# Optimization experiments

Measured on AMD Instinct MI355X. Metric: run time of the kernel, lower is better.

## Reference

```python
import jax, jax.numpy as jnp
import numpy as np

N_NODES = 50000
N_EDGES = 800000
IN_DIM = 128
OUT_DIM = 64
NEG_SLOPE = 0.2
EPS = 1e-8


def setup_inputs() -> dict:
    key = jax.random.key(0)
    k1, k2, k3, k4, k5 = jax.random.split(key, 5)
    x = jax.random.normal(k1, (N_NODES, IN_DIM), dtype=jnp.float32)
    edge_index = jax.random.randint(k2, (2, N_EDGES), 0, N_NODES, dtype=jnp.int64)
    # xavier-like scale for the linear weight
    W = jax.random.normal(k3, (IN_DIM, OUT_DIM), dtype=jnp.float32) * (1.0 / np.sqrt(IN_DIM))
    att_src = jax.random.normal(k4, (OUT_DIM,), dtype=jnp.float32) * 0.1
    att_dst = jax.random.normal(k5, (OUT_DIM,), dtype=jnp.float32) * 0.1
    bias = jnp.zeros((OUT_DIM,), dtype=jnp.float32)
    return {"x": x, "edge_index": edge_index, "W": W,
            "att_src": att_src, "att_dst": att_dst, "bias": bias}


def reference(x, edge_index, W, att_src, att_dst, bias):
    src, dst = edge_index[0], edge_index[1]
    h = x @ W                                  # (N, F_out)
    h_src = h[src]                             # (E, F_out) gather
    # per-edge score: a_src^T h_i + a_dst^T h_j
    e = h_src @ att_src + h[dst] @ att_dst     # (E,)
    e = jax.nn.leaky_relu(e, NEG_SLOPE)
    alpha = jax.nn.sigmoid(e)
    # per-dst normalization (sigmoid attention, not softmax)
    denom = jax.ops.segment_sum(alpha, dst, num_segments=N_NODES) + EPS  # (N,)
    alpha = alpha / denom[dst]
    msg = h_src * alpha[:, None]               # (E, F_out)
    out = jax.ops.segment_sum(msg, dst, num_segments=N_NODES)  # (N, F_out)
    return out + bias
```

## Files before the change

### kernel.cpp

```cpp
#include <hip/hip_runtime.h>

static constexpr int NN   = 50000;
static constexpr int NE   = 800000;
static constexpr int FIN  = 128;
static constexpr int FOUT = 64;
static constexpr int GEMM_NBLK = (NN + 63) / 64;
static constexpr int CAP  = 64;
static constexpr int NRANGE = 8;
static constexpr int RSZ  = NN / NRANGE;
static constexpr int AGG_NBLK = 2048;

static constexpr int NRG    = 196;
static constexpr int CAPSEG = 5120;
static constexpr int PA_NBLK = 98;
static constexpr int FUSE_NBLK = GEMM_NBLK + NRG;

static constexpr int WT_LD = 136;

typedef short bf16x8 __attribute__((ext_vector_type(8)));
typedef float f32x4  __attribute__((ext_vector_type(4)));

static __device__ __forceinline__ unsigned short f2bf(float f) {
    unsigned u = __float_as_uint(f);
    u += 0x7FFFu + ((u >> 16) & 1u);
    return (unsigned short)(u >> 16);
}
static __device__ __forceinline__ float bf2f(unsigned short b) {
    return __uint_as_float(((unsigned)b) << 16);
}

__global__ __launch_bounds__(1024) void k_binA(
    const int* __restrict__ src, const int* __restrict__ dst,
    int* __restrict__ rangeCursor, unsigned int* __restrict__ epack)
{
    __shared__ int hist[NRG];
    __shared__ int base[NRG];
    const int t = threadIdx.x;
    for (int i = t; i < NRG; i += 1024) hist[i] = 0;
    __syncthreads();

    const int g = blockIdx.x * 1024 + t;
    const bool act = g < NE / 8;
    int dd[8], ss[8], rk[8], bn[8];
    if (act) {
        const int4 d0 = ((const int4*)dst)[g * 2];
        const int4 d1 = ((const int4*)dst)[g * 2 + 1];
        const int4 s0 = ((const int4*)src)[g * 2];
        const int4 s1 = ((const int4*)src)[g * 2 + 1];
        dd[0]=d0.x; dd[1]=d0.y; dd[2]=d0.z; dd[3]=d0.w;
        dd[4]=d1.x; dd[5]=d1.y; dd[6]=d1.z; dd[7]=d1.w;
        ss[0]=s0.x; ss[1]=s0.y; ss[2]=s0.z; ss[3]=s0.w;
        ss[4]=s1.x; ss[5]=s1.y; ss[6]=s1.z; ss[7]=s1.w;
        #pragma unroll
        for (int u = 0; u < 8; ++u) {
            bn[u] = dd[u] >> 8;
            rk[u] = atomicAdd(&hist[bn[u]], 1);
        }
    }
    __syncthreads();
    for (int i = t; i < NRG; i += 1024)
        base[i] = hist[i] ? atomicAdd(&rangeCursor[i], hist[i]) : 0;
    __syncthreads();
    if (act) {
        #pragma unroll
        for (int u = 0; u < 8; ++u) {
            const int pos = base[bn[u]] + rk[u];
            if (pos < CAPSEG)
                epack[bn[u] * CAPSEG + pos] =
                    ((unsigned)dd[u] << 16) | (unsigned)ss[u];
        }
    }
}

__global__ __launch_bounds__(256) void k_gemm_binB(
    const float* __restrict__ x, const float* __restrict__ W,
    const float* __restrict__ att_src, const float* __restrict__ att_dst,
    unsigned short* __restrict__ hb, float* __restrict__ ssrc,
    float* __restrict__ sdst, const int* __restrict__ rangeCursor,
    const unsigned int* __restrict__ epack, int* __restrict__ counts,
    unsigned short* __restrict__ bkt)
{
    __shared__ alignas(16) unsigned short SML[64 * WT_LD + 4 * 1024];
    const int t = threadIdx.x;

    if (blockIdx.x >= GEMM_NBLK) {
        const int r = blockIdx.x - GEMM_NBLK;
        int* cur = (int*)SML;
        cur[t] = 0;
        __syncthreads();
        int nE = rangeCursor[r];
        if (nE > CAPSEG) nE = CAPSEG;
        for (int i = t; i < nE; i += 256) {
            const unsigned p = epack[r * CAPSEG + i];
            const int d16 = (int)(p >> 16);
            const int pos = atomicAdd(&cur[d16 & 255], 1);
            if (pos < CAP)
                bkt[(d16 << 6) + pos] = (unsigned short)(p & 0xFFFFu);
        }
        __syncthreads();
        const int node = (r << 8) + t;
        if (node < NN) counts[node] = cur[t];
        return;
    }

    const float4* W4 = (const float4*)W;
    for (int i = t; i < 2048; i += 256) {
        const float4 w4 = W4[i];
        const int k = i >> 4, n0 = (i & 15) << 2;
        SML[(n0+0) * WT_LD + k] = f2bf(w4.x);
        SML[(n0+1) * WT_LD + k] = f2bf(w4.y);
        SML[(n0+2) * WT_LD + k] = f2bf(w4.z);
        SML[(n0+3) * WT_LD + k] = f2bf(w4.w);
    }
    __syncthreads();

    const int wave  = t >> 6;
    const int lane  = t & 63;
    const int row16 = lane & 15;
    const int kblk  = lane >> 4;
    const int rbase = blockIdx.x * 64 + wave * 16;

    int rowA = rbase + row16; if (rowA >= NN) rowA = NN - 1;
    const float* xrow = x + (size_t)rowA * FIN;

    f32x4 acc0 = {0,0,0,0}, acc1 = {0,0,0,0}, acc2 = {0,0,0,0}, acc3 = {0,0,0,0};

    #pragma unroll
    for (int ks = 0; ks < 4; ++ks) {
        const int k0 = ks * 32 + kblk * 8;
        const float4 xa = *(const float4*)(xrow + k0);
        const float4 xb = *(const float4*)(xrow + k0 + 4);
        bf16x8 af;
        af[0] = (short)f2bf(xa.x); af[1] = (short)f2bf(xa.y);
        af[2] = (short)f2bf(xa.z); af[3] = (short)f2bf(xa.w);
        af[4] = (short)f2bf(xb.x); af[5] = (short)f2bf(xb.y);
        af[6] = (short)f2bf(xb.z); af[7] = (short)f2bf(xb.w);

        const bf16x8 b0 = *(const bf16x8*)(&SML[(0*16 + row16) * WT_LD + k0]);
        const bf16x8 b1 = *(const bf16x8*)(&SML[(1*16 + row16) * WT_LD + k0]);
        const bf16x8 b2 = *(const bf16x8*)(&SML[(2*16 + row16) * WT_LD + k0]);
        const bf16x8 b3 = *(const bf16x8*)(&SML[(3*16 + row16) * WT_LD + k0]);
        acc0 = __builtin_amdgcn_mfma_f32_16x16x32_bf16(af, b0, acc0, 0, 0, 0);
        acc1 = __builtin_amdgcn_mfma_f32_16x16x32_bf16(af, b1, acc1, 0, 0, 0);
        acc2 = __builtin_amdgcn_mfma_f32_16x16x32_bf16(af, b2, acc2, 0, 0, 0);
        acc3 = __builtin_amdgcn_mfma_f32_16x16x32_bf16(af, b3, acc3, 0, 0, 0);
    }

    float as0 = att_src[ 0 + row16], as1 = att_src[16 + row16];
    float as2 = att_src[32 + row16], as3 = att_src[48 + row16];
    float ad0 = att_dst[ 0 + row16], ad1 = att_dst[16 + row16];
    float ad2 = att_dst[32 + row16], ad3 = att_dst[48 + row16];
    #pragma unroll
    for (int reg = 0; reg < 4; ++reg) {
        float p = acc0[reg]*as0 + acc1[reg]*as1 + acc2[reg]*as2 + acc3[reg]*as3;
        float q = acc0[reg]*ad0 + acc1[reg]*ad1 + acc2[reg]*ad2 + acc3[reg]*ad3;
        #pragma unroll
        for (int m = 1; m <= 8; m <<= 1) {
            p += __shfl_xor(p, m, 64);
            q += __shfl_xor(q, m, 64);
        }
        if (row16 == 0) {
            const int r = rbase + kblk * 4 + reg;
            if (r < NN) { ssrc[r] = p; sdst[r] = q; }
        }
    }

    unsigned short* hT = SML + 64 * WT_LD + wave * 1024;
    #pragma unroll
    for (int reg = 0; reg < 4; ++reg) {
        const int rr = (kblk * 4 + reg) * 64;
        hT[rr +  0 + row16] = f2bf(acc0[reg]);
        hT[rr + 16 + row16] = f2bf(acc1[reg]);
        hT[rr + 32 + row16] = f2bf(acc2[reg]);
        hT[rr + 48 + row16] = f2bf(acc3[reg]);
    }
    __syncthreads();
    {
        const int rr = lane >> 2;
        const int cc = (lane & 3) << 4;
        const int grow = rbase + rr;
        if (grow < NN) {
            const uint4 v0 = *(const uint4*)(hT + rr * 64 + cc);
            const uint4 v1 = *(const uint4*)(hT + rr * 64 + cc + 8);
            *(uint4*)(hb + (size_t)grow * FOUT + cc)     = v0;
            *(uint4*)(hb + (size_t)grow * FOUT + cc + 8) = v1;
        }
    }
}

__global__ __launch_bounds__(256) void k_agg(
    const unsigned short* __restrict__ hb, const unsigned short* __restrict__ bkt,
    const int* __restrict__ counts, const float* __restrict__ ssrc,
    const float* __restrict__ sdst, const float* __restrict__ bias,
    float* __restrict__ out)
{
    const int r    = blockIdx.x & 7;
    const int wave = threadIdx.x >> 6;
    const int lane = threadIdx.x & 63;
    const int eq   = lane >> 3;
    const int c8   = lane & 7;
    const int c16  = c8 << 3;
    const int wstride = (AGG_NBLK >> 3) * 4;
    const float4 bLo = *(const float4*)(bias + c16);
    const float4 bHi = *(const float4*)(bias + c16 + 4);

    for (int local = (blockIdx.x >> 3) * 4 + wave; local < RSZ;
         local += 2 * wstride) {
        const int localB = local + wstride;
        const bool hasB  = localB < RSZ;
        const int nA   = r * RSZ + local;
        const int nB   = hasB ? r * RSZ + localB : nA;
        const int offA = nA << 6;
        const int offB = nB << 6;
        int cntA = counts[nA]; if (cntA > CAP) cntA = CAP;
        int cntB = hasB ? counts[nB] : 0; if (cntB > CAP) cntB = CAP;
        const float zdA = sdst[nA];
        const float zdB = sdst[nB];

        float accA[8] = {0,0,0,0,0,0,0,0};
        float accB[8] = {0,0,0,0,0,0,0,0};
        float asumA = 0.f, asumB = 0.f;

        const int nchA = (cntA + 15) >> 4;
        const int nchB = (cntB + 15) >> 4;
        const int nch  = nchA > nchB ? nchA : nchB;

        for (int c = 0; c < nch; ++c) {
            const int s0 = (c << 4) + (eq << 1);
            const unsigned wA = *(const unsigned*)(bkt + offA + s0);
            const unsigned wB = *(const unsigned*)(bkt + offB + s0);
            unsigned a0 = wA & 0xFFFFu, a1 = wA >> 16;
            unsigned b0 = wB & 0xFFFFu, b1 = wB >> 16;
            if (s0     >= cntA) a0 = 0u;
            if (s0 + 1 >= cntA) a1 = 0u;
            if (s0     >= cntB) b0 = 0u;
            if (s0 + 1 >= cntB) b1 = 0u;

            const float zA0 = ssrc[a0], zA1 = ssrc[a1];
            const float zB0 = ssrc[b0], zB1 = ssrc[b1];
            const uint4 hA0 = *(const uint4*)(hb + (size_t)a0 * FOUT + c16);
            const uint4 hA1 = *(const uint4*)(hb + (size_t)a1 * FOUT + c16);
            const uint4 hB0 = *(const uint4*)(hb + (size_t)b0 * FOUT + c16);
            const uint4 hB1 = *(const uint4*)(hb + (size_t)b1 * FOUT + c16);

            float sA0 = zA0 + zdA; sA0 = fmaxf(sA0, 0.2f * sA0);
            float sA1 = zA1 + zdA; sA1 = fmaxf(sA1, 0.2f * sA1);
            float sB0 = zB0 + zdB; sB0 = fmaxf(sB0, 0.2f * sB0);
            float sB1 = zB1 + zdB; sB1 = fmaxf(sB1, 0.2f * sB1);
            const float aA0 = (s0     < cntA) ? 1.f/(1.f+__expf(-sA0)) : 0.f;
            const float aA1 = (s0 + 1 < cntA) ? 1.f/(1.f+__expf(-sA1)) : 0.f;
            const float aB0 = (s0     < cntB) ? 1.f/(1.f+__expf(-sB0)) : 0.f;
            const float aB1 = (s0 + 1 < cntB) ? 1.f/(1.f+__expf(-sB1)) : 0.f;

            const unsigned uA0[4] = {hA0.x, hA0.y, hA0.z, hA0.w};
            const unsigned uA1[4] = {hA1.x, hA1.y, hA1.z, hA1.w};
            const unsigned uB0[4] = {hB0.x, hB0.y, hB0.z, hB0.w};
            const unsigned uB1[4] = {hB1.x, hB1.y, hB1.z, hB1.w};
            #pragma unroll
            for (int k = 0; k < 4; ++k) {
                accA[2*k]   += aA0 * bf2f((unsigned short)(uA0[k] & 0xFFFFu))
                             + aA1 * bf2f((unsigned short)(uA1[k] & 0xFFFFu));
                accA[2*k+1] += aA0 * bf2f((unsigned short)(uA0[k] >> 16))
                             + aA1 * bf2f((unsigned short)(uA1[k] >> 16));
                accB[2*k]   += aB0 * bf2f((unsigned short)(uB0[k] & 0xFFFFu))
                             + aB1 * bf2f((unsigned short)(uB1[k] & 0xFFFFu));
                accB[2*k+1] += aB0 * bf2f((unsigned short)(uB0[k] >> 16))
                             + aB1 * bf2f((unsigned short)(uB1[k] >> 16));
            }
            asumA += aA0 + aA1;
            asumB += aB0 + aB1;
        }

        #pragma unroll
        for (int m = 8; m <= 32; m <<= 1) {
            #pragma unroll
            for (int k = 0; k < 8; ++k) {
                accA[k] += __shfl_xor(accA[k], m, 64);
                accB[k] += __shfl_xor(accB[k], m, 64);
            }
            asumA += __shfl_xor(asumA, m, 64);
            asumB += __shfl_xor(asumB, m, 64);
        }

        if (eq == 0) {
            const float invA = 1.f / (asumA + 1e-8f);
            float4 lo, hi;
            lo.x = accA[0]*invA + bLo.x; lo.y = accA[1]*invA + bLo.y;
            lo.z = accA[2]*invA + bLo.z; lo.w = accA[3]*invA + bLo.w;
            hi.x = accA[4]*invA + bHi.x; hi.y = accA[5]*invA + bHi.y;
            hi.z = accA[6]*invA + bHi.z; hi.w = accA[7]*invA + bHi.w;
            *(float4*)(out + (size_t)nA * FOUT + c16)     = lo;
            *(float4*)(out + (size_t)nA * FOUT + c16 + 4) = hi;
            if (hasB) {
                const float invB = 1.f / (asumB + 1e-8f);
                lo.x = accB[0]*invB + bLo.x; lo.y = accB[1]*invB + bLo.y;
                lo.z = accB[2]*invB + bLo.z; lo.w = accB[3]*invB + bLo.w;
                hi.x = accB[4]*invB + bHi.x; hi.y = accB[5]*invB + bHi.y;
                hi.z = accB[6]*invB + bHi.z; hi.w = accB[7]*invB + bHi.w;
                *(float4*)(out + (size_t)nB * FOUT + c16)     = lo;
                *(float4*)(out + (size_t)nB * FOUT + c16 + 4) = hi;
            }
        }
    }
}

extern "C" void kernel_launch(void* const* d_in, const int* in_sizes, int n_in,
                              void* d_out, int out_size, void* d_ws, size_t ws_size,
                              hipStream_t stream)
{
    const float* x       = (const float*)d_in[0];
    const int*   ei      = (const int*)  d_in[1];
    const float* W       = (const float*)d_in[2];
    const float* att_src = (const float*)d_in[3];
    const float* att_dst = (const float*)d_in[4];
    const float* bias    = (const float*)d_in[5];
    float* out = (float*)d_out;

    unsigned short* hb  = (unsigned short*)d_ws;
    float* ssrc         = (float*)(hb + (size_t)NN * FOUT);
    float* sdst         = ssrc + NN;
    int*   counts       = (int*)(sdst + NN);
    unsigned short* bkt = (unsigned short*)(counts + NN);
    unsigned int* epack = (unsigned int*)(bkt + (size_t)NN * CAP);
    int* rangeCursor    = (int*)(epack + (size_t)NRG * CAPSEG);

    const int* src = ei;
    const int* dst = ei + NE;

    (void)hipMemsetAsync(rangeCursor, 0, NRG * sizeof(int), stream);

    k_binA<<<PA_NBLK, 1024, 0, stream>>>(src, dst, rangeCursor, epack);
    k_gemm_binB<<<FUSE_NBLK, 256, 0, stream>>>(x, W, att_src, att_dst,
                                               hb, ssrc, sdst,
                                               rangeCursor, epack,
                                               counts, bkt);
    k_agg<<<AGG_NBLK, 256, 0, stream>>>(hb, bkt, counts, ssrc, sdst,
                                        bias, out);
}
```

Baseline: 128.9 us.

## Fuse coarse edge binning into GEMM kernel and split fine binning per half-range

The coarse binning pass (binA) now runs as extra blocks inside the GEMM launch instead of the fine binning pass, so it overlaps the dense projection. The fine per-node bucketing (binB) moves to its own kernel and uses two blocks per range, each handling half the destination nodes, which doubles parallelism for that stage. Each binA block handles 1024 edge-groups with 256 threads and re-reads dst from global memory instead of keeping it in registers. Each binB block scans the full range and discards half the entries.

```diff
diff --git a/kernel.cpp b/kernel.cpp
--- a/kernel.cpp
+++ b/kernel.cpp
@@ -12,8 +12,9 @@
 
 static constexpr int NRG    = 196;
 static constexpr int CAPSEG = 5120;
-static constexpr int PA_NBLK = 98;
-static constexpr int FUSE_NBLK = GEMM_NBLK + NRG;
+static constexpr int BA_NBLK = 98;
+static constexpr int L1_NBLK = GEMM_NBLK + BA_NBLK;
+static constexpr int BB_NBLK = NRG * 2;
 
 static constexpr int WT_LD = 136;
 
@@ -29,77 +30,59 @@
     return __uint_as_float(((unsigned)b) << 16);
 }
 
-__global__ __launch_bounds__(1024) void k_binA(
-    const int* __restrict__ src, const int* __restrict__ dst,
-    int* __restrict__ rangeCursor, unsigned int* __restrict__ epack)
-{
-    __shared__ int hist[NRG];
-    __shared__ int base[NRG];
-    const int t = threadIdx.x;
-    for (int i = t; i < NRG; i += 1024) hist[i] = 0;
-    __syncthreads();
-
-    const int g = blockIdx.x * 1024 + t;
-    const bool act = g < NE / 8;
-    int dd[8], ss[8], rk[8], bn[8];
-    if (act) {
-        const int4 d0 = ((const int4*)dst)[g * 2];
-        const int4 d1 = ((const int4*)dst)[g * 2 + 1];
-        const int4 s0 = ((const int4*)src)[g * 2];
-        const int4 s1 = ((const int4*)src)[g * 2 + 1];
-        dd[0]=d0.x; dd[1]=d0.y; dd[2]=d0.z; dd[3]=d0.w;
-        dd[4]=d1.x; dd[5]=d1.y; dd[6]=d1.z; dd[7]=d1.w;
-        ss[0]=s0.x; ss[1]=s0.y; ss[2]=s0.z; ss[3]=s0.w;
-        ss[4]=s1.x; ss[5]=s1.y; ss[6]=s1.z; ss[7]=s1.w;
-        #pragma unroll
-        for (int u = 0; u < 8; ++u) {
-            bn[u] = dd[u] >> 8;
-            rk[u] = atomicAdd(&hist[bn[u]], 1);
-        }
-    }
-    __syncthreads();
-    for (int i = t; i < NRG; i += 1024)
-        base[i] = hist[i] ? atomicAdd(&rangeCursor[i], hist[i]) : 0;
-    __syncthreads();
-    if (act) {
-        #pragma unroll
-        for (int u = 0; u < 8; ++u) {
-            const int pos = base[bn[u]] + rk[u];
-            if (pos < CAPSEG)
-                epack[bn[u] * CAPSEG + pos] =
-                    ((unsigned)dd[u] << 16) | (unsigned)ss[u];
-        }
-    }
-}
-
-__global__ __launch_bounds__(256) void k_gemm_binB(
+__global__ __launch_bounds__(256) void k_gemm_binA(
     const float* __restrict__ x, const float* __restrict__ W,
     const float* __restrict__ att_src, const float* __restrict__ att_dst,
     unsigned short* __restrict__ hb, float* __restrict__ ssrc,
-    float* __restrict__ sdst, const int* __restrict__ rangeCursor,
-    const unsigned int* __restrict__ epack, int* __restrict__ counts,
-    unsigned short* __restrict__ bkt)
+    float* __restrict__ sdst, const int* __restrict__ src,
+    const int* __restrict__ dst, int* __restrict__ rangeCursor,
+    unsigned int* __restrict__ epack)
 {
     __shared__ alignas(16) unsigned short SML[64 * WT_LD + 4 * 1024];
     const int t = threadIdx.x;
 
     if (blockIdx.x >= GEMM_NBLK) {
-        const int r = blockIdx.x - GEMM_NBLK;
-        int* cur = (int*)SML;
-        cur[t] = 0;
+        const int b2 = blockIdx.x - GEMM_NBLK;
+        int* hist = (int*)SML;
+        int* base = hist + 256;
+        for (int i = t; i < NRG; i += 256) hist[i] = 0;
         __syncthreads();
-        int nE = rangeCursor[r];
-        if (nE > CAPSEG) nE = CAPSEG;
-        for (int i = t; i < nE; i += 256) {
-            const unsigned p = epack[r * CAPSEG + i];
-            const int d16 = (int)(p >> 16);
-            const int pos = atomicAdd(&cur[d16 & 255], 1);
-            if (pos < CAP)
-                bkt[(d16 << 6) + pos] = (unsigned short)(p & 0xFFFFu);
+
+        int rk[4][8];
+        #pragma unroll
+        for (int b = 0; b < 4; ++b) {
+            const int gi = b2 * 1024 + b * 256 + t;
+            if (gi >= NE / 8) continue;
+            const int4 d0 = ((const int4*)dst)[gi * 2];
+            const int4 d1 = ((const int4*)dst)[gi * 2 + 1];
+            const int dd[8] = {d0.x,d0.y,d0.z,d0.w,d1.x,d1.y,d1.z,d1.w};
+            #pragma unroll
+            for (int u = 0; u < 8; ++u)
+                rk[b][u] = atomicAdd(&hist[dd[u] >> 8], 1);
         }
         __syncthreads();
-        const int node = (r << 8) + t;
-        if (node < NN) counts[node] = cur[t];
+        if (t < NRG)
+            base[t] = hist[t] ? atomicAdd(&rangeCursor[t], hist[t]) : 0;
+        __syncthreads();
+        #pragma unroll
+        for (int b = 0; b < 4; ++b) {
+            const int gi = b2 * 1024 + b * 256 + t;
+            if (gi >= NE / 8) continue;
+            const int4 d0 = ((const int4*)dst)[gi * 2];
+            const int4 d1 = ((const int4*)dst)[gi * 2 + 1];
+            const int4 s0 = ((const int4*)src)[gi * 2];
+            const int4 s1 = ((const int4*)src)[gi * 2 + 1];
+            const int dd[8] = {d0.x,d0.y,d0.z,d0.w,d1.x,d1.y,d1.z,d1.w};
+            const int ss[8] = {s0.x,s0.y,s0.z,s0.w,s1.x,s1.y,s1.z,s1.w};
+            #pragma unroll
+            for (int u = 0; u < 8; ++u) {
+                const int bn = dd[u] >> 8;
+                const int pos = base[bn] + rk[b][u];
+                if (pos < CAPSEG)
+                    epack[bn * CAPSEG + pos] =
+                        ((unsigned)dd[u] << 16) | (unsigned)ss[u];
+            }
+        }
         return;
     }
 
@@ -186,6 +169,33 @@
             *(uint4*)(hb + (size_t)grow * FOUT + cc + 8) = v1;
         }
     }
+}
+
+__global__ __launch_bounds__(256) void k_binB(
+    const int* __restrict__ rangeCursor, const unsigned int* __restrict__ epack,
+    int* __restrict__ counts, unsigned short* __restrict__ bkt)
+{
+    __shared__ int cur[128];
+    const int t = threadIdx.x;
+    const int r    = blockIdx.x >> 1;
+    const int half = blockIdx.x & 1;
+    if (t < 128) cur[t] = 0;
+    __syncthreads();
+    int nE = rangeCursor[r];
+    if (nE > CAPSEG) nE = CAPSEG;
+    for (int i = t; i < nE; i += 256) {
+        const unsigned p = epack[r * CAPSEG + i];
+        const int d16 = (int)(p >> 16);
+        const int loc = d16 & 255;
+        if ((loc >> 7) == half) {
+            const int pos = atomicAdd(&cur[loc & 127], 1);
+            if (pos < CAP)
+                bkt[(d16 << 6) + pos] = (unsigned short)(p & 0xFFFFu);
+        }
+    }
+    __syncthreads();
+    const int node = (r << 8) + (half << 7) + t;
+    if (t < 128 && node < NN) counts[node] = cur[t];
 }
 
 __global__ __launch_bounds__(256) void k_agg(
@@ -329,11 +339,10 @@
 
     (void)hipMemsetAsync(rangeCursor, 0, NRG * sizeof(int), stream);
 
-    k_binA<<<PA_NBLK, 1024, 0, stream>>>(src, dst, rangeCursor, epack);
-    k_gemm_binB<<<FUSE_NBLK, 256, 0, stream>>>(x, W, att_src, att_dst,
-                                               hb, ssrc, sdst,
-                                               rangeCursor, epack,
-                                               counts, bkt);
+    k_gemm_binA<<<L1_NBLK, 256, 0, stream>>>(x, W, att_src, att_dst,
+                                             hb, ssrc, sdst,
+                                             src, dst, rangeCursor, epack);
+    k_binB<<<BB_NBLK, 256, 0, stream>>>(rangeCursor, epack, counts, bkt);
     k_agg<<<AGG_NBLK, 256, 0, stream>>>(hb, bkt, counts, ssrc, sdst,
                                         bias, out);
 }
```

New measurement: 131.0 us. Within noise of the previous version (+1.6%).

## Precompute quantized edge attention during bucketing and split binning from GEMM

Applied to the files above, without the earlier changes.

Edge bucketing moves out of the fused GEMM kernel into its own kernel that runs after the GEMM. It computes each edge's sigmoid attention from ssrc/sdst there and packs it as a 16-bit fixed-point value next to the source index. The aggregation kernel then no longer gathers ssrc or evaluates exp per edge, but the bucket array doubles in size, an extra launch is added, the binning can no longer overlap the GEMM, and attention weights lose precision through 16-bit quantization.

```diff
diff --git a/kernel.cpp b/kernel.cpp
--- a/kernel.cpp
+++ b/kernel.cpp
@@ -13,7 +13,7 @@
 static constexpr int NRG    = 196;
 static constexpr int CAPSEG = 5120;
 static constexpr int PA_NBLK = 98;
-static constexpr int FUSE_NBLK = GEMM_NBLK + NRG;
+static constexpr int BB_NBLK = NRG * 2;
 
 static constexpr int WT_LD = 136;
 
@@ -72,36 +72,14 @@
     }
 }
 
-__global__ __launch_bounds__(256) void k_gemm_binB(
+__global__ __launch_bounds__(256) void k_gemm(
     const float* __restrict__ x, const float* __restrict__ W,
     const float* __restrict__ att_src, const float* __restrict__ att_dst,
     unsigned short* __restrict__ hb, float* __restrict__ ssrc,
-    float* __restrict__ sdst, const int* __restrict__ rangeCursor,
-    const unsigned int* __restrict__ epack, int* __restrict__ counts,
-    unsigned short* __restrict__ bkt)
+    float* __restrict__ sdst)
 {
     __shared__ alignas(16) unsigned short SML[64 * WT_LD + 4 * 1024];
     const int t = threadIdx.x;
-
-    if (blockIdx.x >= GEMM_NBLK) {
-        const int r = blockIdx.x - GEMM_NBLK;
-        int* cur = (int*)SML;
-        cur[t] = 0;
-        __syncthreads();
-        int nE = rangeCursor[r];
-        if (nE > CAPSEG) nE = CAPSEG;
-        for (int i = t; i < nE; i += 256) {
-            const unsigned p = epack[r * CAPSEG + i];
-            const int d16 = (int)(p >> 16);
-            const int pos = atomicAdd(&cur[d16 & 255], 1);
-            if (pos < CAP)
-                bkt[(d16 << 6) + pos] = (unsigned short)(p & 0xFFFFu);
-        }
-        __syncthreads();
-        const int node = (r << 8) + t;
-        if (node < NN) counts[node] = cur[t];
-        return;
-    }
 
     const float4* W4 = (const float4*)W;
     for (int i = t; i < 2048; i += 256) {
@@ -188,10 +166,53 @@
     }
 }
 
+__global__ __launch_bounds__(256) void k_binB(
+    const int* __restrict__ rangeCursor, const unsigned int* __restrict__ epack,
+    const float* __restrict__ ssrc, const float* __restrict__ sdst,
+    int* __restrict__ counts, unsigned int* __restrict__ bkt4)
+{
+    __shared__ int cur[128];
+    const int t = threadIdx.x;
+    const int r    = blockIdx.x >> 1;
+    const int half = blockIdx.x & 1;
+    if (t < 128) cur[t] = 0;
+    __syncthreads();
+    int nE = rangeCursor[r];
+    if (nE > CAPSEG) nE = CAPSEG;
+
+    for (int i0 = t * 4; i0 < nE; i0 += 1024) {
+        const uint4 pq = *(const uint4*)(epack + r * CAPSEG + i0);
+        const unsigned pp[4] = {pq.x, pq.y, pq.z, pq.w};
+        bool in[4]; int dd[4], ss[4];
+        float zs[4], zd[4];
+        #pragma unroll
+        for (int u = 0; u < 4; ++u) {
+            dd[u] = (int)(pp[u] >> 16);
+            ss[u] = (int)(pp[u] & 0xFFFFu);
+            in[u] = (i0 + u < nE) && (((dd[u] & 255) >> 7) == half);
+            zs[u] = in[u] ? ssrc[ss[u]] : 0.f;
+            zd[u] = in[u] ? sdst[dd[u]] : 0.f;
+        }
+        #pragma unroll
+        for (int u = 0; u < 4; ++u) {
+            if (!in[u]) continue;
+            float z = zs[u] + zd[u];
+            z = fmaxf(z, 0.2f * z);
+            const float a = 1.f / (1.f + __expf(-z));
+            const unsigned au = (unsigned)(a * 65535.f + 0.5f);
+            const int pos = atomicAdd(&cur[dd[u] & 127], 1);
+            if (pos < CAP)
+                bkt4[(dd[u] << 6) + pos] = (au << 16) | (unsigned)ss[u];
+        }
+    }
+    __syncthreads();
+    const int node = (r << 8) + (half << 7) + t;
+    if (t < 128 && node < NN) counts[node] = cur[t];
+}
+
 __global__ __launch_bounds__(256) void k_agg(
-    const unsigned short* __restrict__ hb, const unsigned short* __restrict__ bkt,
-    const int* __restrict__ counts, const float* __restrict__ ssrc,
-    const float* __restrict__ sdst, const float* __restrict__ bias,
+    const unsigned short* __restrict__ hb, const unsigned int* __restrict__ bkt4,
+    const int* __restrict__ counts, const float* __restrict__ bias,
     float* __restrict__ out)
 {
     const int r    = blockIdx.x & 7;
@@ -201,6 +222,7 @@
     const int c8   = lane & 7;
     const int c16  = c8 << 3;
     const int wstride = (AGG_NBLK >> 3) * 4;
+    constexpr float DEQ = 1.f / 65535.f;
     const float4 bLo = *(const float4*)(bias + c16);
     const float4 bHi = *(const float4*)(bias + c16 + 4);
 
@@ -214,8 +236,6 @@
         const int offB = nB << 6;
         int cntA = counts[nA]; if (cntA > CAP) cntA = CAP;
         int cntB = hasB ? counts[nB] : 0; if (cntB > CAP) cntB = CAP;
-        const float zdA = sdst[nA];
-        const float zdB = sdst[nB];
 
         float accA[8] = {0,0,0,0,0,0,0,0};
         float accB[8] = {0,0,0,0,0,0,0,0};
@@ -227,30 +247,19 @@
 
         for (int c = 0; c < nch; ++c) {
             const int s0 = (c << 4) + (eq << 1);
-            const unsigned wA = *(const unsigned*)(bkt + offA + s0);
-            const unsigned wB = *(const unsigned*)(bkt + offB + s0);
-            unsigned a0 = wA & 0xFFFFu, a1 = wA >> 16;
-            unsigned b0 = wB & 0xFFFFu, b1 = wB >> 16;
-            if (s0     >= cntA) a0 = 0u;
-            if (s0 + 1 >= cntA) a1 = 0u;
-            if (s0     >= cntB) b0 = 0u;
-            if (s0 + 1 >= cntB) b1 = 0u;
-
-            const float zA0 = ssrc[a0], zA1 = ssrc[a1];
-            const float zB0 = ssrc[b0], zB1 = ssrc[b1];
+            const uint2 wA = *(const uint2*)(bkt4 + offA + s0);
+            const uint2 wB = *(const uint2*)(bkt4 + offB + s0);
+            const unsigned a0 = wA.x & 0xFFFFu, a1 = wA.y & 0xFFFFu;
+            const unsigned b0 = wB.x & 0xFFFFu, b1 = wB.y & 0xFFFFu;
+            const float aA0 = (s0     < cntA) ? (float)(wA.x >> 16) * DEQ : 0.f;
+            const float aA1 = (s0 + 1 < cntA) ? (float)(wA.y >> 16) * DEQ : 0.f;
+            const float aB0 = (s0     < cntB) ? (float)(wB.x >> 16) * DEQ : 0.f;
+            const float aB1 = (s0 + 1 < cntB) ? (float)(wB.y >> 16) * DEQ : 0.f;
+
             const uint4 hA0 = *(const uint4*)(hb + (size_t)a0 * FOUT + c16);
             const uint4 hA1 = *(const uint4*)(hb + (size_t)a1 * FOUT + c16);
             const uint4 hB0 = *(const uint4*)(hb + (size_t)b0 * FOUT + c16);
             const uint4 hB1 = *(const uint4*)(hb + (size_t)b1 * FOUT + c16);
-
-            float sA0 = zA0 + zdA; sA0 = fmaxf(sA0, 0.2f * sA0);
-            float sA1 = zA1 + zdA; sA1 = fmaxf(sA1, 0.2f * sA1);
-            float sB0 = zB0 + zdB; sB0 = fmaxf(sB0, 0.2f * sB0);
-            float sB1 = zB1 + zdB; sB1 = fmaxf(sB1, 0.2f * sB1);
-            const float aA0 = (s0     < cntA) ? 1.f/(1.f+__expf(-sA0)) : 0.f;
-            const float aA1 = (s0 + 1 < cntA) ? 1.f/(1.f+__expf(-sA1)) : 0.f;
-            const float aB0 = (s0     < cntB) ? 1.f/(1.f+__expf(-sB0)) : 0.f;
-            const float aB1 = (s0 + 1 < cntB) ? 1.f/(1.f+__expf(-sB1)) : 0.f;
 
             const unsigned uA0[4] = {hA0.x, hA0.y, hA0.z, hA0.w};
             const unsigned uA1[4] = {hA1.x, hA1.y, hA1.z, hA1.w};
@@ -320,8 +329,8 @@
     float* ssrc         = (float*)(hb + (size_t)NN * FOUT);
     float* sdst         = ssrc + NN;
     int*   counts       = (int*)(sdst + NN);
-    unsigned short* bkt = (unsigned short*)(counts + NN);
-    unsigned int* epack = (unsigned int*)(bkt + (size_t)NN * CAP);
+    unsigned int* bkt4  = (unsigned int*)(counts + NN);
+    unsigned int* epack = (unsigned int*)(bkt4 + (size_t)NN * CAP);
     int* rangeCursor    = (int*)(epack + (size_t)NRG * CAPSEG);
 
     const int* src = ei;
@@ -330,10 +339,9 @@
     (void)hipMemsetAsync(rangeCursor, 0, NRG * sizeof(int), stream);
 
     k_binA<<<PA_NBLK, 1024, 0, stream>>>(src, dst, rangeCursor, epack);
-    k_gemm_binB<<<FUSE_NBLK, 256, 0, stream>>>(x, W, att_src, att_dst,
-                                               hb, ssrc, sdst,
-                                               rangeCursor, epack,
-                                               counts, bkt);
-    k_agg<<<AGG_NBLK, 256, 0, stream>>>(hb, bkt, counts, ssrc, sdst,
-                                        bias, out);
-}
+    k_gemm<<<GEMM_NBLK, 256, 0, stream>>>(x, W, att_src, att_dst,
+                                          hb, ssrc, sdst);
+    k_binB<<<BB_NBLK, 256, 0, stream>>>(rangeCursor, epack, ssrc, sdst,
+                                        counts, bkt4);
+    k_agg<<<AGG_NBLK, 256, 0, stream>>>(hb, bkt4, counts, bias, out);
+}
```

Result: slower. 134.4 us (+4.2%).
